# Kernel tuning notes

Hardware: AMD Instinct MI355X
Metric: run time of the kernel (lower is better)

The kernel has to match this reference:

```python
import jax, jax.numpy as jnp
import numpy as np


def sparsemax(x, axis=-1):
    axis = axis % x.ndim
    d = x.shape[axis]
    # sort descending along axis
    x_sorted = -jnp.sort(-x, axis=axis)
    x_cum = jnp.cumsum(x_sorted, axis=axis)
    k = jnp.arange(1, d + 1, dtype=x.dtype)
    k_shape = [1] * axis + [d] + [1] * (x.ndim - axis - 1)
    k_exp = k.reshape(k_shape)
    # support size: number of entries satisfying 1 + k*z_sorted > cumsum
    constraint = 1 + k_exp * x_sorted > x_cum
    k_x = jnp.sum(constraint, axis=axis, dtype=jnp.int32)
    k_x = jnp.maximum(k_x, 1)
    idx = jnp.expand_dims(k_x - 1, axis=axis)
    tau_sum = jnp.take_along_axis(x_cum, idx, axis=axis)
    tau = (tau_sum - 1) / idx.astype(x.dtype).__add__(1)  # (tau_sum - 1) / k_x
    out = jax.nn.relu(x - tau.astype(x.dtype))
    out = jnp.where(jnp.isfinite(out), out, jnp.asarray(jnp.nan, dtype=x.dtype))
    return out


def setup_inputs() -> dict:
    key = jax.random.key(0)
    x = jax.random.normal(key, (4096, 8192), dtype=jnp.float32)
    return {"x": x}


def reference(x) -> jnp.ndarray:
    return sparsemax(x, axis=-1)
```

## Files before the change

### kernel.cpp

```cpp
#include <hip/hip_runtime.h>
#include <float.h>


constexpr int D       = 8192;
constexpr int THREADS = 256;
constexpr int F4PT    = D / (THREADS * 4);
constexpr int VPT     = D / THREADS;
constexpr int CAP     = 1024;

typedef float f32x4 __attribute__((ext_vector_type(4)));

__device__ __forceinline__ void block_reduce2(float& a, float& b, float* red) {
    #pragma unroll
    for (int off = 1; off < 64; off <<= 1) {
        a += __shfl_xor(a, off, 64);
        b += __shfl_xor(b, off, 64);
    }
    const int wave = threadIdx.x >> 6;
    const int lane = threadIdx.x & 63;
    __syncthreads();
    if (lane == 0) { red[wave] = a; red[4 + wave] = b; }
    __syncthreads();
    a = (red[0] + red[1]) + (red[2] + red[3]);
    b = (red[4] + red[5]) + (red[6] + red[7]);
}

__global__ __launch_bounds__(THREADS, 4)
void sparsemax_kernel(const float* __restrict__ x, float* __restrict__ out) {
    __shared__ float row[D];
    __shared__ float cands[CAP];
    __shared__ float red[8];
    __shared__ int   cnt;

    const long long r = blockIdx.x;
    const f32x4* __restrict__ xr4 = reinterpret_cast<const f32x4*>(x + r * (long long)D);
    f32x4* __restrict__       or4 = reinterpret_cast<f32x4*>(out + r * (long long)D);
    f32x4* row4 = reinterpret_cast<f32x4*>(row);
    const int tid  = threadIdx.x;
    const int wave = tid >> 6, lane = tid & 63;

    if (tid == 0) cnt = 0;

    float m = -FLT_MAX;
    #pragma unroll
    for (int i = 0; i < F4PT; ++i) {
        f32x4 t = xr4[tid + i * THREADS];
        row4[tid + i * THREADS] = t;
        m = fmaxf(m, fmaxf(fmaxf(t.x, t.y), fmaxf(t.z, t.w)));
    }
    #pragma unroll
    for (int off = 1; off < 64; off <<= 1)
        m = fmaxf(m, __shfl_xor(m, off, 64));
    __syncthreads();
    if (lane == 0) red[wave] = m;
    __syncthreads();
    m = fmaxf(fmaxf(red[0], red[1]), fmaxf(red[2], red[3]));
    const float thr = m - 1.0f;

    #pragma unroll
    for (int j = 0; j < VPT; ++j) {
        float v = row[tid + j * THREADS];
        if (v > thr) {
            int p = atomicAdd(&cnt, 1);
            if (p < CAP) cands[p] = v;
        }
    }
    __syncthreads();
    const int n = cnt;

    float tau;
    if (n <= CAP) {
        float c0 = (tid               < n) ? cands[tid              ] : -FLT_MAX;
        float c1 = (tid +     THREADS < n) ? cands[tid +     THREADS] : -FLT_MAX;
        float c2 = (tid + 2 * THREADS < n) ? cands[tid + 2 * THREADS] : -FLT_MAX;
        float c3 = (tid + 3 * THREADS < n) ? cands[tid + 3 * THREADS] : -FLT_MAX;
        tau = thr;
        float kprev = -1.0f;
        for (int it = 0; it < 32; ++it) {
            float S = 0.f, K = 0.f;
            if (c0 > tau) { S += c0; K += 1.f; }
            if (c1 > tau) { S += c1; K += 1.f; }
            if (c2 > tau) { S += c2; K += 1.f; }
            if (c3 > tau) { S += c3; K += 1.f; }
            block_reduce2(S, K, red);
            tau = (S - 1.f) / K;
            if (K == kprev) break;
            kprev = K;
        }
    } else {
        float s = 0.f, z = 0.f;
        #pragma unroll
        for (int j = 0; j < VPT; ++j) s += row[tid + j * THREADS];
        block_reduce2(s, z, red);
        tau = (s - 1.f) / (float)D;
        float kprev = (float)D;
        for (int it = 0; it < 64; ++it) {
            float S = 0.f, K = 0.f;
            #pragma unroll
            for (int j = 0; j < VPT; ++j) {
                float v = row[tid + j * THREADS];
                if (v > tau) { S += v; K += 1.f; }
            }
            block_reduce2(S, K, red);
            if (K < 0.5f) break;
            tau = (S - 1.f) / K;
            if (K == kprev) break;
            kprev = K;
        }
    }

    #pragma unroll
    for (int i = 0; i < F4PT; ++i) {
        f32x4 t = row4[tid + i * THREADS];
        f32x4 o;
        o.x = fmaxf(t.x - tau, 0.f);
        o.y = fmaxf(t.y - tau, 0.f);
        o.z = fmaxf(t.z - tau, 0.f);
        o.w = fmaxf(t.w - tau, 0.f);
        __builtin_nontemporal_store(o, &or4[tid + i * THREADS]);
    }
}

extern "C" void kernel_launch(void* const* d_in, const int* in_sizes, int n_in,
                              void* d_out, int out_size, void* d_ws, size_t ws_size,
                              hipStream_t stream) {
    const float* x = (const float*)d_in[0];
    float* out = (float*)d_out;
    const int rows = in_sizes[0] / D;
    sparsemax_kernel<<<rows, THREADS, 0, stream>>>(x, out);
}
```

Before: 235.4 us.

## Process one row per wavefront and drop LDS row staging

Each 64-lane wavefront now owns a whole row, so all block-level barriers and LDS reductions are replaced by wave shuffles. The row is no longer staged in LDS; it is re-read from global memory for the candidate scan and the output pass. Candidates are compacted with ballot/popcount instead of LDS atomics. This raises per-wave serial work and global reads, relying on cache hits, in exchange for fewer syncs and much lower LDS use, which allows higher occupancy.

```diff
diff --git a/kernel.cpp b/kernel.cpp
--- a/kernel.cpp
+++ b/kernel.cpp
@@ -2,122 +2,109 @@
 #include <float.h>
 
 
-constexpr int D       = 8192;
+constexpr int D    = 8192;
 constexpr int THREADS = 256;
-constexpr int F4PT    = D / (THREADS * 4);
-constexpr int VPT     = D / THREADS;
-constexpr int CAP     = 1024;
+constexpr int WPB  = THREADS / 64;
+constexpr int F4PW = D / (64 * 4);
+constexpr int CAP  = 256;
 
 typedef float f32x4 __attribute__((ext_vector_type(4)));
 
-__device__ __forceinline__ void block_reduce2(float& a, float& b, float* red) {
+__device__ __forceinline__ void wave_reduce2(float& a, float& b) {
     #pragma unroll
     for (int off = 1; off < 64; off <<= 1) {
         a += __shfl_xor(a, off, 64);
         b += __shfl_xor(b, off, 64);
     }
-    const int wave = threadIdx.x >> 6;
-    const int lane = threadIdx.x & 63;
-    __syncthreads();
-    if (lane == 0) { red[wave] = a; red[4 + wave] = b; }
-    __syncthreads();
-    a = (red[0] + red[1]) + (red[2] + red[3]);
-    b = (red[4] + red[5]) + (red[6] + red[7]);
 }
 
 __global__ __launch_bounds__(THREADS, 4)
-void sparsemax_kernel(const float* __restrict__ x, float* __restrict__ out) {
-    __shared__ float row[D];
-    __shared__ float cands[CAP];
-    __shared__ float red[8];
-    __shared__ int   cnt;
+void sparsemax_kernel(const float* __restrict__ x, float* __restrict__ out,
+                      int rows) {
+    __shared__ float cands[WPB][CAP];
 
-    const long long r = blockIdx.x;
-    const f32x4* __restrict__ xr4 = reinterpret_cast<const f32x4*>(x + r * (long long)D);
-    f32x4* __restrict__       or4 = reinterpret_cast<f32x4*>(out + r * (long long)D);
-    f32x4* row4 = reinterpret_cast<f32x4*>(row);
-    const int tid  = threadIdx.x;
-    const int wave = tid >> 6, lane = tid & 63;
-
-    if (tid == 0) cnt = 0;
+    const int wave = threadIdx.x >> 6;
+    const int lane = threadIdx.x & 63;
+    const long long row = (long long)blockIdx.x * WPB + wave;
+    if (row >= rows) return;
+    const f32x4* __restrict__ xr4 = reinterpret_cast<const f32x4*>(x + row * D);
+    f32x4* __restrict__       or4 = reinterpret_cast<f32x4*>(out + row * D);
 
     float m = -FLT_MAX;
-    #pragma unroll
-    for (int i = 0; i < F4PT; ++i) {
-        f32x4 t = xr4[tid + i * THREADS];
-        row4[tid + i * THREADS] = t;
+    #pragma unroll 8
+    for (int i = 0; i < F4PW; ++i) {
+        f32x4 t = xr4[lane + i * 64];
         m = fmaxf(m, fmaxf(fmaxf(t.x, t.y), fmaxf(t.z, t.w)));
     }
     #pragma unroll
     for (int off = 1; off < 64; off <<= 1)
         m = fmaxf(m, __shfl_xor(m, off, 64));
-    __syncthreads();
-    if (lane == 0) red[wave] = m;
-    __syncthreads();
-    m = fmaxf(fmaxf(red[0], red[1]), fmaxf(red[2], red[3]));
     const float thr = m - 1.0f;
 
-    #pragma unroll
-    for (int j = 0; j < VPT; ++j) {
-        float v = row[tid + j * THREADS];
-        if (v > thr) {
-            int p = atomicAdd(&cnt, 1);
-            if (p < CAP) cands[p] = v;
+    int n = 0;
+    #pragma unroll 8
+    for (int i = 0; i < F4PW; ++i) {
+        f32x4 t = xr4[lane + i * 64];
+        bool any4 = (t.x > thr) | (t.y > thr) | (t.z > thr) | (t.w > thr);
+        if (__ballot(any4) == 0ull) continue;
+        #pragma unroll
+        for (int j = 0; j < 4; ++j) {
+            float v = t[j];
+            unsigned long long mk = __ballot(v > thr);
+            if (v > thr) {
+                int pos = n + __popcll(mk & ((1ull << lane) - 1ull));
+                if (pos < CAP) cands[wave][pos] = v;
+            }
+            n += __popcll(mk);
         }
     }
-    __syncthreads();
-    const int n = cnt;
 
-    float tau;
+    float tau = thr;
     if (n <= CAP) {
-        float c0 = (tid               < n) ? cands[tid              ] : -FLT_MAX;
-        float c1 = (tid +     THREADS < n) ? cands[tid +     THREADS] : -FLT_MAX;
-        float c2 = (tid + 2 * THREADS < n) ? cands[tid + 2 * THREADS] : -FLT_MAX;
-        float c3 = (tid + 3 * THREADS < n) ? cands[tid + 3 * THREADS] : -FLT_MAX;
-        tau = thr;
+        float c0 = (lane           < n) ? cands[wave][lane          ] : -FLT_MAX;
+        float c1 = (lane +  64     < n) ? cands[wave][lane +  64    ] : -FLT_MAX;
+        float c2 = (lane + 128     < n) ? cands[wave][lane + 128    ] : -FLT_MAX;
+        float c3 = (lane + 192     < n) ? cands[wave][lane + 192    ] : -FLT_MAX;
         float kprev = -1.0f;
-        for (int it = 0; it < 32; ++it) {
+        for (int it = 0; it < 64; ++it) {
             float S = 0.f, K = 0.f;
             if (c0 > tau) { S += c0; K += 1.f; }
             if (c1 > tau) { S += c1; K += 1.f; }
             if (c2 > tau) { S += c2; K += 1.f; }
             if (c3 > tau) { S += c3; K += 1.f; }
-            block_reduce2(S, K, red);
+            wave_reduce2(S, K);
             tau = (S - 1.f) / K;
             if (K == kprev) break;
             kprev = K;
         }
     } else {
-        float s = 0.f, z = 0.f;
-        #pragma unroll
-        for (int j = 0; j < VPT; ++j) s += row[tid + j * THREADS];
-        block_reduce2(s, z, red);
-        tau = (s - 1.f) / (float)D;
-        float kprev = (float)D;
+        float kprev = -1.0f;
         for (int it = 0; it < 64; ++it) {
             float S = 0.f, K = 0.f;
-            #pragma unroll
-            for (int j = 0; j < VPT; ++j) {
-                float v = row[tid + j * THREADS];
-                if (v > tau) { S += v; K += 1.f; }
+            for (int i = 0; i < F4PW; ++i) {
+                f32x4 t = xr4[lane + i * 64];
+                #pragma unroll
+                for (int j = 0; j < 4; ++j) {
+                    float v = t[j];
+                    if (v > tau) { S += v; K += 1.f; }
+                }
             }
-            block_reduce2(S, K, red);
-            if (K < 0.5f) break;
+            wave_reduce2(S, K);
             tau = (S - 1.f) / K;
             if (K == kprev) break;
             kprev = K;
         }
     }
 
-    #pragma unroll
-    for (int i = 0; i < F4PT; ++i) {
-        f32x4 t = row4[tid + i * THREADS];
+    #pragma unroll 8
+    for (int i = 0; i < F4PW; ++i) {
+        f32x4 t = xr4[lane + i * 64];
         f32x4 o;
         o.x = fmaxf(t.x - tau, 0.f);
         o.y = fmaxf(t.y - tau, 0.f);
         o.z = fmaxf(t.z - tau, 0.f);
         o.w = fmaxf(t.w - tau, 0.f);
-        __builtin_nontemporal_store(o, &or4[tid + i * THREADS]);
+        __builtin_nontemporal_store(o, &or4[lane + i * 64]);
     }
 }
 
@@ -127,5 +114,6 @@
     const float* x = (const float*)d_in[0];
     float* out = (float*)d_out;
     const int rows = in_sizes[0] / D;
-    sparsemax_kernel<<<rows, THREADS, 0, stream>>>(x, out);
+    const int blocks = (rows + WPB - 1) / WPB;
+    sparsemax_kernel<<<blocks, THREADS, 0, stream>>>(x, out, rows);
 }
```

Measured after the change: 250.4 us. +6.4%, slower.
